# Kernel tuning notes

Measured on AMD Instinct MI355X. Metric: run time of the kernel, lower is better.

The kernel has to match this reference:

```python
import jax, jax.numpy as jnp
import numpy as np

N_NODES = 100000
N_EDGES = 1000000
F_IN = 5
H = 64
N_LAYERS = 3


def _mlp2(x, w1, b1, w2, b2):
    # Linear -> ReLU -> Linear -> ReLU
    h = jax.nn.relu(x @ w1 + b1)
    return jax.nn.relu(h @ w2 + b2)


def setup_inputs() -> dict:
    key = jax.random.key(0)
    ks = jax.random.split(key, 12)
    s = 0.05
    return {
        "node_features": jax.random.normal(ks[0], (N_NODES, F_IN), jnp.float32),
        "edge_index": jax.random.randint(ks[1], (2, N_EDGES), 0, N_NODES, jnp.int64 if jax.config.jax_enable_x64 else jnp.int32),
        "enc_w1": jax.random.normal(ks[2], (F_IN, H), jnp.float32) * s,
        "enc_b1": jnp.zeros((H,), jnp.float32),
        "enc_w2": jax.random.normal(ks[3], (H, H), jnp.float32) * s,
        "enc_b2": jnp.zeros((H,), jnp.float32),
        "msg_w1": jax.random.normal(ks[4], (N_LAYERS, 2 * H, H), jnp.float32) * s,
        "msg_b1": jnp.zeros((N_LAYERS, H), jnp.float32),
        "msg_w2": jax.random.normal(ks[5], (N_LAYERS, H, H), jnp.float32) * s,
        "msg_b2": jnp.zeros((N_LAYERS, H), jnp.float32),
        "upd_w1": jax.random.normal(ks[6], (N_LAYERS, 2 * H, H), jnp.float32) * s,
        "upd_b1": jnp.zeros((N_LAYERS, H), jnp.float32),
        "upd_w2": jax.random.normal(ks[7], (N_LAYERS, H, H), jnp.float32) * s,
        "upd_b2": jnp.zeros((N_LAYERS, H), jnp.float32),
        "out_w1": jax.random.normal(ks[8], (H, H), jnp.float32) * s,
        "out_b1": jnp.zeros((H,), jnp.float32),
        "out_w2": jax.random.normal(ks[9], (H, 3), jnp.float32) * s,
        "out_b2": jnp.zeros((3,), jnp.float32),
    }


def reference(node_features, edge_index, enc_w1, enc_b1, enc_w2, enc_b2,
              msg_w1, msg_b1, msg_w2, msg_b2,
              upd_w1, upd_b1, upd_w2, upd_b2,
              out_w1, out_b1, out_w2, out_b2):
    n = node_features.shape[0]
    src, dst = edge_index[0], edge_index[1]
    h = _mlp2(node_features, enc_w1, enc_b1, enc_w2, enc_b2)  # [N, H]
    # precompute in-degree counts (constant across layers)
    counts = jax.ops.segment_sum(jnp.ones((src.shape[0],), h.dtype), dst, num_segments=n)
    denom = jnp.maximum(counts, 1.0)[:, None]  # nodes w/o incoming edges -> agg stays zero
    for l in range(N_LAYERS):
        combined = jnp.concatenate([h[src], h[dst]], axis=-1)  # [E, 2H]
        m = _mlp2(combined, msg_w1[l], msg_b1[l], msg_w2[l], msg_b2[l])  # [E, H]
        agg = jax.ops.segment_sum(m, dst, num_segments=n) / denom  # scatter-mean by dst
        h = _mlp2(jnp.concatenate([h, agg], axis=-1), upd_w1[l], upd_b1[l], upd_w2[l], upd_b2[l])
    pred = jax.nn.relu(h @ out_w1 + out_b1) @ out_w2 + out_b2  # [N, 3]
    return 2.0 * jnp.pi * jax.nn.sigmoid(pred)
```

## Files before the change

### kernel.cpp

```cpp
#include <hip/hip_runtime.h>
#include <math.h>

#define NN 100000
#define NE 1000000
#define H 64
#define EB 128
#define MBT 256
#define MSTRIDE 130
#define NSH 8

typedef _Float16 f16x8 __attribute__((ext_vector_type(8)));
typedef _Float16 f16x2 __attribute__((ext_vector_type(2)));
typedef float f32x4  __attribute__((ext_vector_type(4)));

static __device__ __forceinline__ float relu_(float x){ return fmaxf(x, 0.0f); }

static __device__ __forceinline__ unsigned short f2h_(float f){
  union { _Float16 h; unsigned short u; } x; x.h = (_Float16)f; return x.u;
}
static __device__ __forceinline__ float h2f_(unsigned short u){
  union { unsigned short u; _Float16 h; } x; x.u = u; return (float)x.h;
}
static __device__ __forceinline__ unsigned int pkh_(float lo, float hi){
  union { f16x2 v; unsigned int u; } x;
  x.v[0] = (_Float16)lo; x.v[1] = (_Float16)hi;
  return x.u;
}
static __device__ __forceinline__ unsigned int addrelu2_(unsigned int a, unsigned int b){
  union { unsigned int u; f16x2 v; } x, y, r;
  x.u = a; y.u = b;
  f16x2 s = x.v + y.v;
  _Float16 z = (_Float16)0.0f;
  r.v[0] = (s[0] > z) ? s[0] : z;
  r.v[1] = (s[1] > z) ? s[1] : z;
  return r.u;
}
static __device__ __forceinline__ unsigned int mulpk_(unsigned int a, f16x2 s){
  union { unsigned int u; f16x2 v; } x;
  x.u = a; x.v = x.v * s;
  return x.u;
}
static __device__ __forceinline__ void fma32(float* o, float a, const float* wr){
  #pragma unroll
  for (int j=0;j<32;j++) o[j] = fmaf(a, wr[j], o[j]);
}

__global__ __launch_bounds__(256, 2) void enc_full_kernel(
    const float* __restrict__ x,
    const float* __restrict__ w1, const float* __restrict__ b1,
    const float* __restrict__ w2, const float* __restrict__ b2,
    unsigned short* __restrict__ hbf)
{
  int v = blockIdx.x*256 + threadIdx.x;
  if (v >= NN) return;
  float in0[5];
  #pragma unroll
  for (int k=0;k<5;k++) in0[k] = x[(size_t)v*5 + k];
  float o[64];
  #pragma unroll
  for (int j=0;j<64;j++) o[j] = b2[j];
  #pragma unroll 4
  for (int k=0;k<64;k++){
    float tk = b1[k];
    #pragma unroll
    for (int kk=0;kk<5;kk++) tk = fmaf(in0[kk], w1[kk*H + k], tk);
    tk = relu_(tk);
    const float* wr = w2 + k*H;
    #pragma unroll
    for (int j=0;j<64;j++) o[j] = fmaf(tk, wr[j], o[j]);
  }
  unsigned int u[32];
  #pragma unroll
  for (int j=0;j<32;j++) u[j] = pkh_(relu_(o[2*j]), relu_(o[2*j+1]));
  uint4* dp = (uint4*)(hbf + (size_t)v*H);
  #pragma unroll
  for (int j=0;j<8;j++) dp[j] = *(uint4*)&u[4*j];
}

__global__ __launch_bounds__(256) void rank_kernel(const int* __restrict__ dst,
                                                   int* __restrict__ counts8,
                                                   int* __restrict__ rank)
{
  int t = blockIdx.x*256 + threadIdx.x;
  int e0 = t*4;
  int* cs = counts8 + (size_t)(blockIdx.x & (NSH-1))*NN;
  if (e0 + 3 < NE){
    int4 d4 = *(const int4*)(dst + e0);
    int r0 = atomicAdd(&cs[d4.x], 1);
    int r1 = atomicAdd(&cs[d4.y], 1);
    int r2 = atomicAdd(&cs[d4.z], 1);
    int r3 = atomicAdd(&cs[d4.w], 1);
    *(int4*)(rank + e0) = make_int4(r0, r1, r2, r3);
  } else {
    for (int e = e0; e < NE; ++e) rank[e] = atomicAdd(&cs[dst[e]], 1);
  }
}

__global__ __launch_bounds__(1024) void scan1_kernel(const int* __restrict__ counts8,
                                                     int* __restrict__ counts,
                                                     int* __restrict__ pfx,
                                                     int* __restrict__ row_excl,
                                                     int* __restrict__ part)
{
  __shared__ int wsum[16];
  int tid = threadIdx.x;
  int i = blockIdx.x*1024 + tid;
  int v = 0;
  if (i < NN){
    int run = 0;
    #pragma unroll
    for (int sh=0; sh<NSH; sh++){
      int c = counts8[(size_t)sh*NN + i];
      pfx[(size_t)sh*NN + i] = run;
      run += c;
    }
    v = run;
    counts[i] = run;
  }
  int lane = tid & 63, w = tid >> 6;
  int s = v;
  #pragma unroll
  for (int off=1; off<64; off<<=1){
    int t = __shfl_up(s, off, 64);
    if (lane >= off) s += t;
  }
  if (lane == 63) wsum[w] = s;
  __syncthreads();
  if (w == 0 && lane < 16){
    int t = wsum[lane];
    #pragma unroll
    for (int off=1; off<16; off<<=1){
      int u = __shfl_up(t, off, 64);
      if (lane >= off) t += u;
    }
    wsum[lane] = t;
  }
  __syncthreads();
  int base = (w > 0) ? wsum[w-1] : 0;
  int incl = base + s;
  if (i < NN) row_excl[i] = incl - v;
  if (tid == 1023) part[blockIdx.x] = incl;
}

__global__ __launch_bounds__(128) void scan2_kernel(int* __restrict__ part, int nparts)
{
  __shared__ int buf[128];
  int tid = threadIdx.x;
  int v = (tid < nparts) ? part[tid] : 0;
  buf[tid] = v;
  __syncthreads();
  for (int off=1; off<128; off<<=1){
    int t = (tid >= off) ? buf[tid-off] : 0;
    __syncthreads();
    buf[tid] += t;
    __syncthreads();
  }
  if (tid < nparts) part[tid] = buf[tid] - v;
}

__global__ __launch_bounds__(256) void fill_kernel(
    const int* __restrict__ src, const int* __restrict__ dst,
    const int* __restrict__ row_excl, const int* __restrict__ part,
    const int* __restrict__ pfx,
    const int* __restrict__ rank, int2* __restrict__ sedge)
{
  int e = blockIdx.x*256 + threadIdx.x;
  if (e >= NE) return;
  int d = dst[e];
  int sh = (e >> 10) & (NSH-1);
  int p = row_excl[d] + part[d >> 10] + pfx[(size_t)sh*NN + d] + rank[e];
  sedge[p] = make_int2(src[e], d);
}

__global__ __launch_bounds__(256) void count_kernel(const int* __restrict__ dst,
                                                    int* __restrict__ counts)
{
  int e = blockIdx.x*256 + threadIdx.x;
  if (e < NE) atomicAdd(&counts[dst[e]], 1);
}

__global__ __launch_bounds__(256) void prep_all_kernel(
    const float* __restrict__ uw1, const float* __restrict__ uw2,
    const float* __restrict__ mw1, const float* __restrict__ mw2,
    const float* __restrict__ ow1, unsigned short* __restrict__ wp)
{
  int i = blockIdx.x*256 + threadIdx.x;
  if (i >= 77824) return;
  float val;
  if (i < 24576){
    int l = i / 8192, r = i & 8191;
    int j = r & 7, col = (r >> 3) & 63, g = r >> 9;
    int k = (g >> 2)*32 + (g & 3)*8 + j;
    val = uw1[(size_t)l*8192 + k*64 + col];
  } else if (i < 36864){
    int t = i - 24576; int l = t / 4096, r = t & 4095;
    int j = r & 7, col = (r >> 3) & 63, g = r >> 9;
    int k = (g >> 2)*32 + (g & 3)*8 + j;
    val = uw2[(size_t)l*4096 + k*64 + col];
  } else if (i < 61440){
    int t = i - 36864; int l = t / 8192, r = t & 8191;
    int j = r & 7, col = (r >> 3) & 127, g = r >> 10;
    int k = (g >> 2)*32 + (g & 3)*8 + j;
    val = mw1[(size_t)l*8192 + ((col >> 6)*64 + k)*64 + (col & 63)];
  } else if (i < 65536){
    int r = i - 61440;
    int j = r & 7, col = (r >> 3) & 63, g = r >> 9;
    int k = (g >> 2)*32 + (g & 3)*8 + j;
    val = ow1[k*64 + col];
  } else {
    int t = i - 65536; int l = t / 4096, r = t & 4095;
    int j = r & 7, col = (r >> 3) & 63, g = r >> 9;
    int k = (g >> 2)*32 + (g & 3)*8 + j;
    val = mw2[(size_t)l*4096 + k*64 + col];
  }
  wp[i] = f2h_(val);
}

__global__ __launch_bounds__(MBT, 4) void msg_mfma_kernel(
    const unsigned short* __restrict__ P,
    const unsigned short* __restrict__ w2p,
    const float* __restrict__ b2,
    const int2* __restrict__ sedge,
    unsigned short* __restrict__ aggh,
    float* __restrict__ bval, int* __restrict__ bdst)
{
  __shared__ unsigned short mlds[64*MSTRIDE];
  __shared__ int2 sdl[EB];
  const int tid  = threadIdx.x;
  const int wave = tid >> 6, lane = tid & 63, quad = lane >> 4, c = lane & 15;

  int bid = blockIdx.x;
  int ng = gridDim.x >> 3;
  int lb = (bid < (ng << 3)) ? ((bid & 7)*ng + (bid >> 3)) : bid;
  const int base = lb*EB;

  if (tid < EB){
    int p = base + tid;
    int2 sv = make_int2(0, -1);
    if (p < NE) sv = sedge[p];
    sdl[tid] = sv;
  }

  f16x8 bfr[4][2];
  #pragma unroll
  for (int n=0;n<4;n++)
    #pragma unroll
    for (int kb=0;kb<2;kb++)
      bfr[n][kb] = *(const f16x8*)(w2p + (((kb*4 + quad)*64 + n*16 + c) << 3));
  float bv[4];
  #pragma unroll
  for (int n=0;n<4;n++) bv[n] = b2[n*16 + c];

  __syncthreads();

  const int ebase = wave*32;
  #pragma unroll
  for (int t=0;t<2;t++){
    int2 sd = sdl[ebase + t*16 + c];
    int s = sd.x;
    int d = sd.y < 0 ? 0 : sd.y;
    const unsigned short* p1 = P + (size_t)s*128 + quad*8;
    const unsigned short* p2 = P + (size_t)d*128 + 64 + quad*8;
    f16x8 af[2];
    #pragma unroll
    for (int kb=0;kb<2;kb++){
      uint4 u1 = *(const uint4*)(p1 + kb*32);
      uint4 u2 = *(const uint4*)(p2 + kb*32);
      union { unsigned int u[4]; f16x8 v; } A;
      A.u[0] = addrelu2_(u1.x, u2.x);
      A.u[1] = addrelu2_(u1.y, u2.y);
      A.u[2] = addrelu2_(u1.z, u2.z);
      A.u[3] = addrelu2_(u1.w, u2.w);
      af[kb] = A.v;
    }

    f32x4 acc4[4];
    #pragma unroll
    for (int n=0;n<4;n++) acc4[n] = (f32x4){0.f, 0.f, 0.f, 0.f};
    #pragma unroll
    for (int n=0;n<4;n++){
      acc4[n] = __builtin_amdgcn_mfma_f32_16x16x32_f16(af[0], bfr[n][0], acc4[n], 0, 0, 0);
      acc4[n] = __builtin_amdgcn_mfma_f32_16x16x32_f16(af[1], bfr[n][1], acc4[n], 0, 0, 0);
    }

    int e0 = ebase + t*16 + quad*4;
    #pragma unroll
    for (int n=0;n<4;n++){
      int ch = n*16 + c;
      float v0 = relu_(acc4[n][0] + bv[n]);
      float v1 = relu_(acc4[n][1] + bv[n]);
      float v2 = relu_(acc4[n][2] + bv[n]);
      float v3 = relu_(acc4[n][3] + bv[n]);
      *(unsigned int*)&mlds[ch*MSTRIDE + e0]     = pkh_(v0, v1);
      *(unsigned int*)&mlds[ch*MSTRIDE + e0 + 2] = pkh_(v2, v3);
    }
  }
  __syncthreads();

  {
    const int g = wave;
    const int ch = lane;
    int dA  = sdl[lane].y;
    int dAm = (lane == 0) ? ~dA : sdl[lane-1].y;
    unsigned long long m0 = __ballot(dA != dAm);
    int dB  = sdl[64+lane].y;
    int dBm = sdl[63+lane].y;
    unsigned long long m1 = __ballot(dB != dBm);

    auto isb = [&](int p)->bool{
      return (p < 64) ? ((m0 >> p) & 1ull) : ((m1 >> (p-64)) & 1ull);
    };
    auto nextb = [&](int p)->int{
      int q = p + 1;
      if (q < 64){
        unsigned long long t = m0 >> q;
        if (t) return q + __builtin_ctzll(t);
        q = 64;
      }
      int off = q - 64;
      if (off < 64){
        unsigned long long t = m1 >> off;
        if (t) return q + __builtin_ctzll(t);
      }
      return EB;
    };

    int r = g*32;
    if (g > 0 && !isb(r)) r = nextb(r);
    const int myEnd = (g+1)*32;
    while (r < myEnd){
      int nb = nextb(r);
      int cur = sdl[r].y;
      float s2 = 0.f;
      for (int rr = r; rr < nb; ++rr)
        s2 += h2f_(mlds[ch*MSTRIDE + rr]);
      if (cur >= 0){
        bool headB = (r == 0);
        bool tailB = (nb == EB);
        if (headB){
          bval[(size_t)(2*lb)*64 + ch] = s2;
          if (ch == 0) bdst[2*lb] = cur;
          if (tailB){
            bval[(size_t)(2*lb+1)*64 + ch] = 0.f;
            if (ch == 0) bdst[2*lb+1] = cur;
          }
        } else if (tailB){
          bval[(size_t)(2*lb+1)*64 + ch] = s2;
          if (ch == 0) bdst[2*lb+1] = cur;
        } else {
          aggh[(size_t)cur*H + ch] = f2h_(s2);
        }
      }
      r = nb;
    }
  }
}

#define BW 16
__global__ __launch_bounds__(256) void bnd_fixup_kernel(
    const int* __restrict__ bdst, const float* __restrict__ bval,
    unsigned short* __restrict__ aggh, int nbnd)
{
  const int wave = threadIdx.x >> 6, ch = threadIdx.x & 63;
  int g = blockIdx.x*4 + wave;
  int r0 = g*BW;
  if (r0 >= nbnd) return;
  int r = r0;
  if (r0 > 0){
    int prev = bdst[r0-1];
    while (r < nbnd && bdst[r] == prev) r++;
  }
  int rlim = r0 + BW;
  while (r < nbnd){
    int runstart = r;
    if (runstart >= rlim) break;
    int cur = bdst[r];
    float s = 0.f;
    while (r < nbnd && bdst[r] == cur){
      s += bval[(size_t)r*64 + ch];
      r++;
    }
    if (cur >= 0) aggh[(size_t)cur*H + ch] = f2h_(s);
  }
}

__global__ __launch_bounds__(256) void node_fused_kernel(
    const unsigned short* __restrict__ hbf,
    const unsigned short* __restrict__ aggh, const int* __restrict__ counts,
    const unsigned short* __restrict__ uw1p, const float* __restrict__ ub1,
    const unsigned short* __restrict__ uw2p, const float* __restrict__ ub2,
    const unsigned short* __restrict__ w3p,  const float* __restrict__ b3,
    const float* __restrict__ ow2, const float* __restrict__ ob2,
    unsigned short* __restrict__ hout,
    unsigned short* __restrict__ Pout,
    float* __restrict__ outp,
    int mode)
{
  __shared__ __align__(16) unsigned short act[64*72];
  __shared__ __align__(16) unsigned short pst[64*136];
  const int tid = threadIdx.x, wave = tid >> 6, lane = tid & 63;
  const int quad = lane >> 4, c = lane & 15;
  const int vb = blockIdx.x*64;
  int myv = vb + wave*16 + c;
  int vld = myv < NN ? myv : NN-1;

  if (mode != 2){
    int cntv = counts[vld];
    float invf = (cntv > 0) ? (1.0f / (float)cntv) : 0.0f;
    f16x2 invd2; invd2[0] = (_Float16)invf; invd2[1] = (_Float16)invf;
    f16x8 a1[4];
    a1[0] = *(const f16x8*)(hbf + (size_t)vld*H + quad*8);
    a1[1] = *(const f16x8*)(hbf + (size_t)vld*H + 32 + quad*8);
    #pragma unroll
    for (int kb2=0; kb2<2; kb2++){
      uint4 u = *(const uint4*)(aggh + (size_t)vld*H + kb2*32 + quad*8);
      union { unsigned int u[4]; f16x8 v; } A;
      A.u[0] = mulpk_(u.x, invd2);
      A.u[1] = mulpk_(u.y, invd2);
      A.u[2] = mulpk_(u.z, invd2);
      A.u[3] = mulpk_(u.w, invd2);
      a1[2+kb2] = A.v;
    }
    f32x4 acc1[4];
    #pragma unroll
    for (int n=0;n<4;n++) acc1[n] = (f32x4){0.f,0.f,0.f,0.f};
    #pragma unroll
    for (int n=0;n<4;n++){
      #pragma unroll
      for (int kb=0;kb<4;kb++){
        f16x8 b = *(const f16x8*)(uw1p + (((kb*4 + quad)*64 + n*16 + c) << 3));
        acc1[n] = __builtin_amdgcn_mfma_f32_16x16x32_f16(a1[kb], b, acc1[n], 0, 0, 0);
      }
    }
    #pragma unroll
    for (int n=0;n<4;n++){
      float bb = ub1[n*16 + c];
      #pragma unroll
      for (int r=0;r<4;r++)
        act[(wave*16 + quad*4 + r)*72 + n*16 + c] = f2h_(relu_(acc1[n][r] + bb));
    }

    f16x8 a2[2];
    a2[0] = *(const f16x8*)(act + (wave*16 + c)*72 + quad*8);
    a2[1] = *(const f16x8*)(act + (wave*16 + c)*72 + 32 + quad*8);
    f32x4 acc2[4];
    #pragma unroll
    for (int n=0;n<4;n++) acc2[n] = (f32x4){0.f,0.f,0.f,0.f};
    #pragma unroll
    for (int n=0;n<4;n++){
      #pragma unroll
      for (int kb=0;kb<2;kb++){
        f16x8 b = *(const f16x8*)(uw2p + (((kb*4 + quad)*64 + n*16 + c) << 3));
        acc2[n] = __builtin_amdgcn_mfma_f32_16x16x32_f16(a2[kb], b, acc2[n], 0, 0, 0);
      }
    }
    #pragma unroll
    for (int n=0;n<4;n++){
      float bb = ub2[n*16 + c];
      #pragma unroll
      for (int r=0;r<4;r++)
        act[(wave*16 + quad*4 + r)*72 + n*16 + c] = f2h_(relu_(acc2[n][r] + bb));
    }
  }

  f16x8 a3[2];
  if (mode == 2){
    a3[0] = *(const f16x8*)(hbf + (size_t)vld*H + quad*8);
    a3[1] = *(const f16x8*)(hbf + (size_t)vld*H + 32 + quad*8);
  } else {
    a3[0] = *(const f16x8*)(act + (wave*16 + c)*72 + quad*8);
    a3[1] = *(const f16x8*)(act + (wave*16 + c)*72 + 32 + quad*8);
  }

  if (mode == 1){
    f32x4 acc3[4];
    #pragma unroll
    for (int n=0;n<4;n++) acc3[n] = (f32x4){0.f,0.f,0.f,0.f};
    #pragma unroll
    for (int n=0;n<4;n++){
      #pragma unroll
      for (int kb=0;kb<2;kb++){
        f16x8 b = *(const f16x8*)(w3p + (((kb*4 + quad)*64 + n*16 + c) << 3));
        acc3[n] = __builtin_amdgcn_mfma_f32_16x16x32_f16(a3[kb], b, acc3[n], 0, 0, 0);
      }
    }
    #pragma unroll
    for (int n=0;n<4;n++){
      float bb = b3[n*16 + c];
      #pragma unroll
      for (int r=0;r<4;r++)
        act[(wave*16 + quad*4 + r)*72 + n*16 + c] = f2h_(relu_(acc3[n][r] + bb));
    }
  } else {
    f32x4 acc3[8];
    #pragma unroll
    for (int n=0;n<8;n++) acc3[n] = (f32x4){0.f,0.f,0.f,0.f};
    #pragma unroll
    for (int n=0;n<8;n++){
      #pragma unroll
      for (int kb=0;kb<2;kb++){
        f16x8 b = *(const f16x8*)(w3p + (((kb*4 + quad)*128 + n*16 + c) << 3));
        acc3[n] = __builtin_amdgcn_mfma_f32_16x16x32_f16(a3[kb], b, acc3[n], 0, 0, 0);
      }
    }
    #pragma unroll
    for (int n=0;n<8;n++){
      int ch = n*16 + c;
      float bb = (ch >= 64) ? b3[ch - 64] : 0.0f;
      #pragma unroll
      for (int r=0;r<4;r++)
        pst[(wave*16 + quad*4 + r)*136 + ch] = f2h_(acc3[n][r] + bb);
    }
  }

  __syncthreads();

  if (mode == 0){
    #pragma unroll
    for (int rr=0; rr<2; rr++){
      int idx = tid + rr*256;
      int node = idx >> 3, ko = (idx & 7)*8;
      int v = vb + node;
      if (v < NN) *(uint4*)(hout + (size_t)v*H + ko) = *(const uint4*)(act + node*72 + ko);
    }
  }
  if (mode == 0 || mode == 2){
    #pragma unroll
    for (int rr=0; rr<4; rr++){
      int idx = tid + rr*256;
      int node = idx >> 4, cho = (idx & 15)*8;
      int v = vb + node;
      if (v < NN) *(uint4*)(Pout + (size_t)v*128 + cho) = *(const uint4*)(pst + node*136 + cho);
    }
  }
  if (mode == 1){
    if (tid < 192){
      int node = tid / 3;
      int v = vb + node;
      if (v < NN){
        int cm = tid - node*3;
        float s = ob2[cm];
        #pragma unroll 8
        for (int k=0;k<64;k++)
          s = fmaf(h2f_(act[node*72 + k]), ow2[k*3 + cm], s);
        outp[(size_t)v*3 + cm] = 6.283185307179586f / (1.0f + __expf(-s));
      }
    }
  }
}

__global__ __launch_bounds__(256) void enc_kernel_legacy(
    const float* __restrict__ x,
    const float* __restrict__ w1, const float* __restrict__ b1,
    const float* __restrict__ w2, const float* __restrict__ b2,
    float* __restrict__ h)
{
  int v = blockIdx.x*256 + threadIdx.x;
  if (v >= NN) return;
  float in0[5];
  #pragma unroll
  for (int k=0;k<5;k++) in0[k] = x[v*5+k];
  float hid[H];
  #pragma unroll
  for (int j=0;j<H;j++) hid[j] = b1[j];
  #pragma unroll
  for (int k=0;k<5;k++){
    #pragma unroll
    for (int j=0;j<H;j++) hid[j] = fmaf(in0[k], w1[k*H+j], hid[j]);
  }
  float o[H];
  #pragma unroll
  for (int j=0;j<H;j++) o[j] = b2[j];
  #pragma unroll
  for (int k=0;k<H;k++){
    float hk = relu_(hid[k]);
    #pragma unroll
    for (int j=0;j<H;j++) o[j] = fmaf(hk, w2[k*H+j], o[j]);
  }
  float4* hw = (float4*)(h + (size_t)v*H);
  #pragma unroll
  for (int j4=0;j4<H/4;j4++){
    float4 t;
    t.x = relu_(o[4*j4+0]); t.y = relu_(o[4*j4+1]);
    t.z = relu_(o[4*j4+2]); t.w = relu_(o[4*j4+3]);
    hw[j4] = t;
  }
}

__global__ __launch_bounds__(256) void msg_kernel_atomic(
    const float* __restrict__ h,
    const int* __restrict__ src, const int* __restrict__ dst,
    const float* __restrict__ w1, const float* __restrict__ b1,
    const float* __restrict__ w2, const float* __restrict__ b2,
    float* __restrict__ agg)
{
  int e = blockIdx.x*256 + threadIdx.x;
  if (e >= NE) return;
  int s = src[e], d = dst[e];
  const float4* hs = (const float4*)(h + (size_t)s*H);
  const float4* hd = (const float4*)(h + (size_t)d*H);
  float hid[H];
  #pragma unroll
  for (int j=0;j<H;j++) hid[j] = b1[j];
  #pragma unroll 4
  for (int k4=0;k4<16;k4++){
    float4 a = hs[k4];
    const float* wr = w1 + (size_t)(4*k4)*H;
    #pragma unroll
    for (int j=0;j<H;j++) hid[j] = fmaf(a.x, wr[j], hid[j]);
    #pragma unroll
    for (int j=0;j<H;j++) hid[j] = fmaf(a.y, wr[H+j], hid[j]);
    #pragma unroll
    for (int j=0;j<H;j++) hid[j] = fmaf(a.z, wr[2*H+j], hid[j]);
    #pragma unroll
    for (int j=0;j<H;j++) hid[j] = fmaf(a.w, wr[3*H+j], hid[j]);
  }
  #pragma unroll 4
  for (int k4=0;k4<16;k4++){
    float4 a = hd[k4];
    const float* wr = w1 + (size_t)(64 + 4*k4)*H;
    #pragma unroll
    for (int j=0;j<H;j++) hid[j] = fmaf(a.x, wr[j], hid[j]);
    #pragma unroll
    for (int j=0;j<H;j++) hid[j] = fmaf(a.y, wr[H+j], hid[j]);
    #pragma unroll
    for (int j=0;j<H;j++) hid[j] = fmaf(a.z, wr[2*H+j], hid[j]);
    #pragma unroll
    for (int j=0;j<H;j++) hid[j] = fmaf(a.w, wr[3*H+j], hid[j]);
  }
  float o[H];
  #pragma unroll
  for (int j=0;j<H;j++) o[j] = b2[j];
  #pragma unroll
  for (int k=0;k<H;k++){
    float hk = relu_(hid[k]);
    #pragma unroll
    for (int j=0;j<H;j++) o[j] = fmaf(hk, w2[k*H+j], o[j]);
  }
  float* arow = agg + (size_t)d*H;
  #pragma unroll
  for (int j=0;j<H;j++) atomicAdd(arow + j, relu_(o[j]));
}

__global__ __launch_bounds__(256) void div_kernel(float* __restrict__ agg,
                                                  const int* __restrict__ counts)
{
  int i = blockIdx.x*256 + threadIdx.x;
  if (i >= NN*H/4) return;
  int v = i / (H/4);
  float invd = 1.0f / fmaxf((float)counts[v], 1.0f);
  float4* a = (float4*)agg + i;
  float4 t = *a;
  t.x *= invd; t.y *= invd; t.z *= invd; t.w *= invd;
  *a = t;
}

__global__ __launch_bounds__(256) void upd_kernel_legacy(
    float* __restrict__ h, const float* __restrict__ agg,
    const float* __restrict__ w1, const float* __restrict__ b1,
    const float* __restrict__ w2, const float* __restrict__ b2)
{
  int v = blockIdx.x*256 + threadIdx.x;
  if (v >= NN) return;
  const float4* hv = (const float4*)(h + (size_t)v*H);
  const float4* av = (const float4*)(agg + (size_t)v*H);
  float hid[H];
  #pragma unroll
  for (int j=0;j<H;j++) hid[j] = b1[j];
  #pragma unroll 4
  for (int k4=0;k4<16;k4++){
    float4 a = hv[k4];
    const float* wr = w1 + (size_t)(4*k4)*H;
    #pragma unroll
    for (int j=0;j<H;j++) hid[j] = fmaf(a.x, wr[j], hid[j]);
    #pragma unroll
    for (int j=0;j<H;j++) hid[j] = fmaf(a.y, wr[H+j], hid[j]);
    #pragma unroll
    for (int j=0;j<H;j++) hid[j] = fmaf(a.z, wr[2*H+j], hid[j]);
    #pragma unroll
    for (int j=0;j<H;j++) hid[j] = fmaf(a.w, wr[3*H+j], hid[j]);
  }
  #pragma unroll 4
  for (int k4=0;k4<16;k4++){
    float4 a = av[k4];
    const float* wr = w1 + (size_t)(64 + 4*k4)*H;
    #pragma unroll
    for (int j=0;j<H;j++) hid[j] = fmaf(a.x, wr[j], hid[j]);
    #pragma unroll
    for (int j=0;j<H;j++) hid[j] = fmaf(a.y, wr[H+j], hid[j]);
    #pragma unroll
    for (int j=0;j<H;j++) hid[j] = fmaf(a.z, wr[2*H+j], hid[j]);
    #pragma unroll
    for (int j=0;j<H;j++) hid[j] = fmaf(a.w, wr[3*H+j], hid[j]);
  }
  float o[H];
  #pragma unroll
  for (int j=0;j<H;j++) o[j] = b2[j];
  #pragma unroll
  for (int k=0;k<H;k++){
    float hk = relu_(hid[k]);
    #pragma unroll
    for (int j=0;j<H;j++) o[j] = fmaf(hk, w2[k*H+j], o[j]);
  }
  float4* hw = (float4*)(h + (size_t)v*H);
  #pragma unroll
  for (int j4=0;j4<H/4;j4++){
    float4 t;
    t.x = relu_(o[4*j4+0]); t.y = relu_(o[4*j4+1]);
    t.z = relu_(o[4*j4+2]); t.w = relu_(o[4*j4+3]);
    hw[j4] = t;
  }
}

__global__ __launch_bounds__(256) void out_kernel2(
    const float* __restrict__ h,
    const float* __restrict__ w1, const float* __restrict__ b1,
    const float* __restrict__ w2, const float* __restrict__ b2,
    float* __restrict__ out)
{
  int v = blockIdx.x*256 + threadIdx.x;
  if (v >= NN) return;
  const float4* hv = (const float4*)(h + (size_t)v*H);
  float pr[3] = { b2[0], b2[1], b2[2] };
  #pragma unroll 1
  for (int half=0; half<2; half++){
    float o[32];
    #pragma unroll
    for (int j=0;j<32;j++) o[j] = b1[half*32 + j];
    #pragma unroll 4
    for (int k4=0;k4<16;k4++){
      float4 a = hv[k4];
      const float* wr = w1 + (4*k4)*H + half*32;
      fma32(o, a.x, wr); fma32(o, a.y, wr+H); fma32(o, a.z, wr+2*H); fma32(o, a.w, wr+3*H);
    }
    #pragma unroll
    for (int j=0;j<32;j++){
      float hk = relu_(o[j]);
      int k = half*32 + j;
      pr[0] = fmaf(hk, w2[k*3+0], pr[0]);
      pr[1] = fmaf(hk, w2[k*3+1], pr[1]);
      pr[2] = fmaf(hk, w2[k*3+2], pr[2]);
    }
  }
  #pragma unroll
  for (int c=0;c<3;c++)
    out[(size_t)v*3 + c] = 6.283185307179586f / (1.0f + __expf(-pr[c]));
}


extern "C" void kernel_launch(void* const* d_in, const int* in_sizes, int n_in,
                              void* d_out, int out_size, void* d_ws, size_t ws_size,
                              hipStream_t stream)
{
  const float* x      = (const float*)d_in[0];
  const int*   ei     = (const int*)  d_in[1];
  const float* enc_w1 = (const float*)d_in[2];
  const float* enc_b1 = (const float*)d_in[3];
  const float* enc_w2 = (const float*)d_in[4];
  const float* enc_b2 = (const float*)d_in[5];
  const float* msg_w1 = (const float*)d_in[6];
  const float* msg_b1 = (const float*)d_in[7];
  const float* msg_w2 = (const float*)d_in[8];
  const float* msg_b2 = (const float*)d_in[9];
  const float* upd_w1 = (const float*)d_in[10];
  const float* upd_b1 = (const float*)d_in[11];
  const float* upd_w2 = (const float*)d_in[12];
  const float* upd_b2 = (const float*)d_in[13];
  const float* out_w1 = (const float*)d_in[14];
  const float* out_b1 = (const float*)d_in[15];
  const float* out_w2 = (const float*)d_in[16];
  const float* out_b2 = (const float*)d_in[17];
  float* out = (float*)d_out;

  const int* srcp = ei;
  const int* dstp = ei + NE;

  const int nodeBlocks  = (NN + 255)/256;
  const int edgeBlocks  = (NE + 255)/256;
  const int rankBlocks  = (NE + 1023)/1024;
  const int msgBlocks   = (NE + EB - 1)/EB;
  const int nbnd        = 2*msgBlocks;
  const int fixBlocks   = ((nbnd + BW - 1)/BW + 3)/4;
  const int scanBlocks  = (NN + 1023)/1024;
  const int fusedBlocks = (NN + 63)/64;

  char* wp_ = (char*)d_ws;
  auto take = [&wp_](size_t bytes) -> char* {
    char* r = wp_;
    wp_ += (bytes + 255) & ~(size_t)255;
    return r;
  };
  unsigned short* hbf = (unsigned short*)take((size_t)NN*H*sizeof(unsigned short));
  unsigned short* P   = (unsigned short*)take((size_t)NN*128*sizeof(unsigned short));
  unsigned short* aggh= (unsigned short*)take((size_t)NN*H*sizeof(unsigned short));
  int* counts         = (int*)take((size_t)NN*sizeof(int));
  int* counts8        = (int*)take((size_t)NSH*NN*sizeof(int));
  int* pfx            = (int*)take((size_t)NSH*NN*sizeof(int));
  int* row_excl       = (int*)take((size_t)NN*sizeof(int));
  int* part           = (int*)take(1024);
  int* rank           = (int*)take((size_t)NE*sizeof(int));
  int2* sedge         = (int2*)take((size_t)NE*sizeof(int2));
  float* bval         = (float*)take((size_t)nbnd*64*sizeof(float));
  int* bdst           = (int*)take((size_t)nbnd*sizeof(int));
  unsigned short* wpz = (unsigned short*)take((size_t)77824*sizeof(unsigned short));
  size_t need = (size_t)(wp_ - (char*)d_ws);

  const size_t UW1 = 0, UW2 = 24576, PPJ = 36864, OW1 = 61440, MW2 = 65536;

  if (ws_size >= need) {
    (void)hipMemsetAsync(counts8, 0, (size_t)NSH*NN*sizeof(int), stream);
    (void)hipMemsetAsync(bdst, 0xFF, nbnd*sizeof(int), stream);

    enc_full_kernel<<<nodeBlocks, 256, 0, stream>>>(x, enc_w1, enc_b1, enc_w2, enc_b2, hbf);

    rank_kernel<<<rankBlocks, 256, 0, stream>>>(dstp, counts8, rank);
    scan1_kernel<<<scanBlocks, 1024, 0, stream>>>(counts8, counts, pfx, row_excl, part);
    scan2_kernel<<<1, 128, 0, stream>>>(part, scanBlocks);
    fill_kernel<<<edgeBlocks, 256, 0, stream>>>(srcp, dstp, row_excl, part, pfx, rank, sedge);
    prep_all_kernel<<<(77824 + 255)/256, 256, 0, stream>>>(upd_w1, upd_w2, msg_w1, msg_w2, out_w1, wpz);

    node_fused_kernel<<<fusedBlocks, 256, 0, stream>>>(
        hbf, aggh, counts,
        nullptr, nullptr, nullptr, nullptr,
        wpz + PPJ, msg_b1, nullptr, nullptr,
        nullptr, P, nullptr, 2);

    for (int l=0; l<3; l++){
      msg_mfma_kernel<<<msgBlocks, MBT, 0, stream>>>(P, wpz + MW2 + (size_t)l*4096,
          msg_b2 + (size_t)l*H, sedge, aggh, bval, bdst);
      bnd_fixup_kernel<<<fixBlocks, 256, 0, stream>>>(bdst, bval, aggh, nbnd);
      if (l < 2){
        node_fused_kernel<<<fusedBlocks, 256, 0, stream>>>(
            hbf, aggh, counts,
            wpz + UW1 + (size_t)l*8192, upd_b1 + (size_t)l*H,
            wpz + UW2 + (size_t)l*4096, upd_b2 + (size_t)l*H,
            wpz + PPJ + (size_t)(l+1)*8192, msg_b1 + (size_t)(l+1)*H,
            nullptr, nullptr,
            hbf, P, nullptr, 0);
      } else {
        node_fused_kernel<<<fusedBlocks, 256, 0, stream>>>(
            hbf, aggh, counts,
            wpz + UW1 + (size_t)l*8192, upd_b1 + (size_t)l*H,
            wpz + UW2 + (size_t)l*4096, upd_b2 + (size_t)l*H,
            wpz + OW1, out_b1,
            out_w2, out_b2,
            nullptr, nullptr, out, 1);
      }
    }
  } else {
    char* fp = (char*)d_ws;
    float* fh   = (float*)fp;  fp += (size_t)NN*H*sizeof(float);
    float* fagg = (float*)fp;  fp += (size_t)NN*H*sizeof(float);
    int* fcnt   = (int*)fp;

    (void)hipMemsetAsync(fcnt, 0, NN*sizeof(int), stream);
    enc_kernel_legacy<<<nodeBlocks, 256, 0, stream>>>(x, enc_w1, enc_b1, enc_w2, enc_b2, fh);
    count_kernel<<<edgeBlocks, 256, 0, stream>>>(dstp, fcnt);
    for (int l=0; l<3; l++){
      (void)hipMemsetAsync(fagg, 0, (size_t)NN*H*sizeof(float), stream);
      msg_kernel_atomic<<<edgeBlocks, 256, 0, stream>>>(fh, srcp, dstp,
          msg_w1 + (size_t)l*128*H, msg_b1 + (size_t)l*H,
          msg_w2 + (size_t)l*H*H,   msg_b2 + (size_t)l*H, fagg);
      div_kernel<<<(NN*H/4 + 255)/256, 256, 0, stream>>>(fagg, fcnt);
      upd_kernel_legacy<<<nodeBlocks, 256, 0, stream>>>(fh, fagg,
          upd_w1 + (size_t)l*128*H, upd_b1 + (size_t)l*H,
          upd_w2 + (size_t)l*H*H,   upd_b2 + (size_t)l*H);
    }
    out_kernel2<<<nodeBlocks, 256, 0, stream>>>(fh, out_w1, out_b1, out_w2, out_b2, out);
  }
}
```

Before: 401.7 us.

## Replace boundary fixup kernel with packed f16 atomics and double edge block

Segments that straddle a message-block boundary are now combined with global packed-f16 atomic adds straight into the aggregate buffer. This removes the separate boundary-fixup kernel and its float staging buffers. The edge block doubles from 128 to 256 edges per workgroup, which roughly halves the number of boundary segments. In exchange, the aggregate buffer has to be zeroed with a memset before each layer, and f16 atomic accumulation adds rounding error and makes the summation order nondeterministic.

```diff
diff --git a/kernel.cpp b/kernel.cpp
--- a/kernel.cpp
+++ b/kernel.cpp
@@ -4,9 +4,9 @@
 #define NN 100000
 #define NE 1000000
 #define H 64
-#define EB 128
+#define EB 256
 #define MBT 256
-#define MSTRIDE 130
+#define MSTRIDE 258
 #define NSH 8
 
 typedef _Float16 f16x8 __attribute__((ext_vector_type(8)));
@@ -39,6 +39,9 @@
   union { unsigned int u; f16x2 v; } x;
   x.u = a; x.v = x.v * s;
   return x.u;
+}
+static __device__ __forceinline__ void atomic_pk_f16_(unsigned short* p, unsigned int pk){
+  asm volatile("global_atomic_pk_add_f16 %0, %1, off" :: "v"(p), "v"(pk) : "memory");
 }
 static __device__ __forceinline__ void fma32(float* o, float a, const float* wr){
   #pragma unroll
@@ -221,8 +224,7 @@
     const unsigned short* __restrict__ w2p,
     const float* __restrict__ b2,
     const int2* __restrict__ sedge,
-    unsigned short* __restrict__ aggh,
-    float* __restrict__ bval, int* __restrict__ bdst)
+    unsigned short* __restrict__ aggh)
 {
   __shared__ unsigned short mlds[64*MSTRIDE];
   __shared__ int2 sdl[EB];
@@ -253,9 +255,9 @@
 
   __syncthreads();
 
-  const int ebase = wave*32;
-  #pragma unroll
-  for (int t=0;t<2;t++){
+  const int ebase = wave*64;
+  #pragma unroll
+  for (int t=0;t<4;t++){
     int2 sd = sdl[ebase + t*16 + c];
     int s = sd.x;
     int d = sd.y < 0 ? 0 : sd.y;
@@ -300,15 +302,22 @@
   {
     const int g = wave;
     const int ch = lane;
-    int dA  = sdl[lane].y;
-    int dAm = (lane == 0) ? ~dA : sdl[lane-1].y;
-    unsigned long long m0 = __ballot(dA != dAm);
-    int dB  = sdl[64+lane].y;
-    int dBm = sdl[63+lane].y;
-    unsigned long long m1 = __ballot(dB != dBm);
+    unsigned long long m0, m1, m2, m3;
+    {
+      int dA, dAm;
+      dA = sdl[lane].y;        dAm = (lane == 0) ? ~dA : sdl[lane-1].y;
+      m0 = __ballot(dA != dAm);
+      dA = sdl[64+lane].y;     dAm = sdl[63+lane].y;
+      m1 = __ballot(dA != dAm);
+      dA = sdl[128+lane].y;    dAm = sdl[127+lane].y;
+      m2 = __ballot(dA != dAm);
+      dA = sdl[192+lane].y;    dAm = sdl[191+lane].y;
+      m3 = __ballot(dA != dAm);
+    }
 
     auto isb = [&](int p)->bool{
-      return (p < 64) ? ((m0 >> p) & 1ull) : ((m1 >> (p-64)) & 1ull);
+      unsigned long long mm = (p < 64) ? m0 : (p < 128) ? m1 : (p < 192) ? m2 : m3;
+      return (mm >> (p & 63)) & 1ull;
     };
     auto nextb = [&](int p)->int{
       int q = p + 1;
@@ -317,17 +326,26 @@
         if (t) return q + __builtin_ctzll(t);
         q = 64;
       }
-      int off = q - 64;
-      if (off < 64){
-        unsigned long long t = m1 >> off;
+      if (q < 128){
+        unsigned long long t = m1 >> (q - 64);
+        if (t) return q + __builtin_ctzll(t);
+        q = 128;
+      }
+      if (q < 192){
+        unsigned long long t = m2 >> (q - 128);
+        if (t) return q + __builtin_ctzll(t);
+        q = 192;
+      }
+      if (q < 256){
+        unsigned long long t = m3 >> (q - 192);
         if (t) return q + __builtin_ctzll(t);
       }
       return EB;
     };
 
-    int r = g*32;
+    int r = g*64;
     if (g > 0 && !isb(r)) r = nextb(r);
-    const int myEnd = (g+1)*32;
+    const int myEnd = (g+1)*64;
     while (r < myEnd){
       int nb = nextb(r);
       int cur = sdl[r].y;
@@ -335,52 +353,19 @@
       for (int rr = r; rr < nb; ++rr)
         s2 += h2f_(mlds[ch*MSTRIDE + rr]);
       if (cur >= 0){
-        bool headB = (r == 0);
-        bool tailB = (nb == EB);
-        if (headB){
-          bval[(size_t)(2*lb)*64 + ch] = s2;
-          if (ch == 0) bdst[2*lb] = cur;
-          if (tailB){
-            bval[(size_t)(2*lb+1)*64 + ch] = 0.f;
-            if (ch == 0) bdst[2*lb+1] = cur;
+        bool bnd = (r == 0) || (nb == EB);
+        if (bnd){
+          float other = __shfl_xor(s2, 1);
+          if ((ch & 1) == 0){
+            unsigned int pk = pkh_(s2, other);
+            atomic_pk_f16_(aggh + (size_t)cur*H + ch, pk);
           }
-        } else if (tailB){
-          bval[(size_t)(2*lb+1)*64 + ch] = s2;
-          if (ch == 0) bdst[2*lb+1] = cur;
         } else {
           aggh[(size_t)cur*H + ch] = f2h_(s2);
         }
       }
       r = nb;
     }
-  }
-}
-
-#define BW 16
-__global__ __launch_bounds__(256) void bnd_fixup_kernel(
-    const int* __restrict__ bdst, const float* __restrict__ bval,
-    unsigned short* __restrict__ aggh, int nbnd)
-{
-  const int wave = threadIdx.x >> 6, ch = threadIdx.x & 63;
-  int g = blockIdx.x*4 + wave;
-  int r0 = g*BW;
-  if (r0 >= nbnd) return;
-  int r = r0;
-  if (r0 > 0){
-    int prev = bdst[r0-1];
-    while (r < nbnd && bdst[r] == prev) r++;
-  }
-  int rlim = r0 + BW;
-  while (r < nbnd){
-    int runstart = r;
-    if (runstart >= rlim) break;
-    int cur = bdst[r];
-    float s = 0.f;
-    while (r < nbnd && bdst[r] == cur){
-      s += bval[(size_t)r*64 + ch];
-      r++;
-    }
-    if (cur >= 0) aggh[(size_t)cur*H + ch] = f2h_(s);
   }
 }
 
@@ -779,8 +764,6 @@
   const int edgeBlocks  = (NE + 255)/256;
   const int rankBlocks  = (NE + 1023)/1024;
   const int msgBlocks   = (NE + EB - 1)/EB;
-  const int nbnd        = 2*msgBlocks;
-  const int fixBlocks   = ((nbnd + BW - 1)/BW + 3)/4;
   const int scanBlocks  = (NN + 1023)/1024;
   const int fusedBlocks = (NN + 63)/64;
 
@@ -800,8 +783,6 @@
   int* part           = (int*)take(1024);
   int* rank           = (int*)take((size_t)NE*sizeof(int));
   int2* sedge         = (int2*)take((size_t)NE*sizeof(int2));
-  float* bval         = (float*)take((size_t)nbnd*64*sizeof(float));
-  int* bdst           = (int*)take((size_t)nbnd*sizeof(int));
   unsigned short* wpz = (unsigned short*)take((size_t)77824*sizeof(unsigned short));
   size_t need = (size_t)(wp_ - (char*)d_ws);
 
@@ -809,7 +790,6 @@
 
   if (ws_size >= need) {
     (void)hipMemsetAsync(counts8, 0, (size_t)NSH*NN*sizeof(int), stream);
-    (void)hipMemsetAsync(bdst, 0xFF, nbnd*sizeof(int), stream);
 
     enc_full_kernel<<<nodeBlocks, 256, 0, stream>>>(x, enc_w1, enc_b1, enc_w2, enc_b2, hbf);
 
@@ -826,9 +806,9 @@
         nullptr, P, nullptr, 2);
 
     for (int l=0; l<3; l++){
+      (void)hipMemsetAsync(aggh, 0, (size_t)NN*H*sizeof(unsigned short), stream);
       msg_mfma_kernel<<<msgBlocks, MBT, 0, stream>>>(P, wpz + MW2 + (size_t)l*4096,
-          msg_b2 + (size_t)l*H, sedge, aggh, bval, bdst);
-      bnd_fixup_kernel<<<fixBlocks, 256, 0, stream>>>(bdst, bval, aggh, nbnd);
+          msg_b2 + (size_t)l*H, sedge, aggh);
       if (l < 2){
         node_fused_kernel<<<fusedBlocks, 256, 0, stream>>>(
             hbf, aggh, counts,
```

After: 401.6 us. About the same (-0.0%).
